# Performance work log

Hardware: AMD Instinct MI355X
Metric: run time of the kernel (lower is better)

## Reference

```python
import jax, jax.numpy as jnp
from jax import lax
import numpy as np

B, T, F, H, O = 4096, 2048, 8, 32, 8


def setup_inputs() -> dict:
    key = jax.random.key(0)
    k = jax.random.split(key, 7)
    s = 1.0 / np.sqrt(H).astype(np.float32)  # torch RNN/Linear init bound
    x = jax.random.normal(k[0], (B, T, F), dtype=jnp.float32)
    W_ih = jax.random.uniform(k[1], (H, F), minval=-s, maxval=s, dtype=jnp.float32)
    W_hh = jax.random.uniform(k[2], (H, H), minval=-s, maxval=s, dtype=jnp.float32)
    b_ih = jax.random.uniform(k[3], (H,), minval=-s, maxval=s, dtype=jnp.float32)
    b_hh = jax.random.uniform(k[4], (H,), minval=-s, maxval=s, dtype=jnp.float32)
    W_out = jax.random.uniform(k[5], (O, H), minval=-s, maxval=s, dtype=jnp.float32)
    b_out = jax.random.uniform(k[6], (O,), minval=-s, maxval=s, dtype=jnp.float32)
    return {"x": x, "W_ih": W_ih, "W_hh": W_hh, "b_ih": b_ih, "b_hh": b_hh,
            "W_out": W_out, "b_out": b_out}


def reference(x, W_ih, W_hh, b_ih, b_hh, W_out, b_out):
    # Precompute input projection for all timesteps: [B, T, H]
    xp = jnp.einsum('btf,hf->bth', x, W_ih) + b_ih + b_hh
    h0 = jnp.zeros((x.shape[0], W_hh.shape[0]), dtype=x.dtype)

    def step(h, xt):  # xt: [B, H]
        h = jnp.tanh(xt + h @ W_hh.T)
        return h, None

    h_final, _ = lax.scan(step, h0, jnp.swapaxes(xp, 0, 1))  # scan over T
    # torch returns out(h) with h of shape [num_layers=1, B, H]
    y = h_final @ W_out.T + b_out  # [B, O]
    return y[None]  # [1, B, O]
```

## Files before the change

### kernel.cpp

```cpp
#include <hip/hip_runtime.h>


typedef float v2f __attribute__((ext_vector_type(2)));

static constexpr int T_STEPS = 2048;
static constexpr int FDIM    = 8;
static constexpr int HDIM    = 32;
static constexpr int ODIM    = 8;
static constexpr int ROWS_PER_BLOCK = 8;
static constexpr int GROUP   = 4;
static constexpr int NGROUP  = T_STEPS / GROUP;
static constexpr int LSTR    = 36;

__global__ __launch_bounds__(256, 2) void rnn_scan_kernel(
    const float* __restrict__ x,
    const float* __restrict__ W_ih,
    const float* __restrict__ W_hh,
    const float* __restrict__ b_ih,
    const float* __restrict__ b_hh,
    const float* __restrict__ W_out,
    const float* __restrict__ b_out,
    float* __restrict__ out)
{
    const float K = 2.8853900817779268f;
    const int tid  = threadIdx.x;
    const int lane = tid & 63;
    const int wave = tid >> 6;
    const int q    = lane & 31;
    const int sub  = lane >> 5;
    const int r    = wave * 2 + sub;
    const long long b = (long long)blockIdx.x * ROWS_PER_BLOCK + r;

    __shared__ float hsh[ROWS_PER_BLOCK][LSTR];

    v2f wh[16];
    const float* whr = W_hh + q * HDIM;
#pragma unroll
    for (int i = 0; i < 16; ++i) {
        v2f w; w[0] = whr[2 * i] * K; w[1] = whr[2 * i + 1] * K; wh[i] = w;
    }
    v2f wiv[4];
    const float* wir = W_ih + q * FDIM;
#pragma unroll
    for (int i = 0; i < 4; ++i) {
        v2f w; w[0] = wir[2 * i] * K; w[1] = wir[2 * i + 1] * K; wiv[i] = w;
    }
    const float bias = (b_ih[q] + b_hh[q]) * K;

    hsh[r][q] = 0.0f;

    const float4* xq = reinterpret_cast<const float4*>(x + (size_t)b * T_STEPS * FDIM);
    const float4* hp = reinterpret_cast<const float4*>(&hsh[r][0]);
    float* hw = &hsh[r][q];

#define LOADG(buf, gi)                                                         \
    {                                                                          \
        const int base = (gi) * (2 * GROUP);                                   \
        _Pragma("unroll")                                                      \
        for (int k = 0; k < 2 * GROUP; ++k) buf[k] = xq[base + k];             \
    }                                                                          \
    asm volatile("" ::: "memory");

#define STEP(xa, xb)                                                           \
    {                                                                          \
        float4 g0 = hp[0], g1 = hp[1], g2 = hp[2], g3 = hp[3];                 \
        float4 g4 = hp[4], g5 = hp[5], g6 = hp[6], g7 = hp[7];                 \
        v2f a0; a0[0] = bias; a0[1] = 0.0f;                                    \
        v2f a1 = {0.0f, 0.0f}, a2 = {0.0f, 0.0f}, a3 = {0.0f, 0.0f};           \
        v2f t;                                                                 \
        t[0] = xa.x; t[1] = xa.y;  a0 = __builtin_elementwise_fma(wiv[0], t, a0); \
        t[0] = xa.z; t[1] = xa.w;  a1 = __builtin_elementwise_fma(wiv[1], t, a1); \
        t[0] = xb.x; t[1] = xb.y;  a2 = __builtin_elementwise_fma(wiv[2], t, a2); \
        t[0] = xb.z; t[1] = xb.w;  a3 = __builtin_elementwise_fma(wiv[3], t, a3); \
        t[0] = g0.x; t[1] = g0.y;  a0 = __builtin_elementwise_fma(wh[0],  t, a0); \
        t[0] = g0.z; t[1] = g0.w;  a1 = __builtin_elementwise_fma(wh[1],  t, a1); \
        t[0] = g1.x; t[1] = g1.y;  a2 = __builtin_elementwise_fma(wh[2],  t, a2); \
        t[0] = g1.z; t[1] = g1.w;  a3 = __builtin_elementwise_fma(wh[3],  t, a3); \
        t[0] = g2.x; t[1] = g2.y;  a0 = __builtin_elementwise_fma(wh[4],  t, a0); \
        t[0] = g2.z; t[1] = g2.w;  a1 = __builtin_elementwise_fma(wh[5],  t, a1); \
        t[0] = g3.x; t[1] = g3.y;  a2 = __builtin_elementwise_fma(wh[6],  t, a2); \
        t[0] = g3.z; t[1] = g3.w;  a3 = __builtin_elementwise_fma(wh[7],  t, a3); \
        t[0] = g4.x; t[1] = g4.y;  a0 = __builtin_elementwise_fma(wh[8],  t, a0); \
        t[0] = g4.z; t[1] = g4.w;  a1 = __builtin_elementwise_fma(wh[9],  t, a1); \
        t[0] = g5.x; t[1] = g5.y;  a2 = __builtin_elementwise_fma(wh[10], t, a2); \
        t[0] = g5.z; t[1] = g5.w;  a3 = __builtin_elementwise_fma(wh[11], t, a3); \
        t[0] = g6.x; t[1] = g6.y;  a0 = __builtin_elementwise_fma(wh[12], t, a0); \
        t[0] = g6.z; t[1] = g6.w;  a1 = __builtin_elementwise_fma(wh[13], t, a1); \
        t[0] = g7.x; t[1] = g7.y;  a2 = __builtin_elementwise_fma(wh[14], t, a2); \
        t[0] = g7.z; t[1] = g7.w;  a3 = __builtin_elementwise_fma(wh[15], t, a3); \
        v2f s01 = a0 + a1, s23 = a2 + a3;                                      \
        v2f st  = s01 + s23;                                                   \
        float s = st[0] + st[1];                                               \
        float e = __builtin_amdgcn_exp2f(s);                                   \
        float rc = __builtin_amdgcn_rcpf(e + 1.0f);                            \
        *hw = fmaf(-2.0f, rc, 1.0f);                                           \
    }

#define STEPS(buf)                                                             \
    STEP(buf[0], buf[1]) STEP(buf[2], buf[3])                                  \
    STEP(buf[4], buf[5]) STEP(buf[6], buf[7])

    float4 bufA[2 * GROUP], bufB[2 * GROUP];
    LOADG(bufA, 0)

    for (int g = 0; g < NGROUP; g += 2) {
        LOADG(bufB, g + 1)
        STEPS(bufA)
        {
            const int gn = (g + 2 < NGROUP) ? (g + 2) : (NGROUP - 1);
            LOADG(bufA, gn)
        }
        STEPS(bufB)
    }
#undef STEPS
#undef STEP
#undef LOADG

    __syncthreads();
    if (tid < ROWS_PER_BLOCK * ODIM) {
        const int rr = tid >> 3;
        const int o  = tid & 7;
        float acc = b_out[o];
#pragma unroll
        for (int j = 0; j < HDIM; ++j)
            acc = fmaf(hsh[rr][j], W_out[o * HDIM + j], acc);
        out[((long long)blockIdx.x * ROWS_PER_BLOCK + rr) * ODIM + o] = acc;
    }
}

extern "C" void kernel_launch(void* const* d_in, const int* in_sizes, int n_in,
                              void* d_out, int out_size, void* d_ws, size_t ws_size,
                              hipStream_t stream) {
    const float* x     = (const float*)d_in[0];
    const float* W_ih  = (const float*)d_in[1];
    const float* W_hh  = (const float*)d_in[2];
    const float* b_ih  = (const float*)d_in[3];
    const float* b_hh  = (const float*)d_in[4];
    const float* W_out = (const float*)d_in[5];
    const float* b_out = (const float*)d_in[6];

    const int B = in_sizes[0] / (T_STEPS * FDIM);
    const int grid = B / ROWS_PER_BLOCK;

    rnn_scan_kernel<<<grid, 256, 0, stream>>>(
        x, W_ih, W_hh, b_ih, b_hh, W_out, b_out, (float*)d_out);
}
```

Baseline: 687.0 us.

## Use fp16 hidden state with fdot2 and split-K lanes with swizzle reduction

Stores the hidden state in LDS as fp16 and computes the recurrent matvec with packed fp16 dot2 instructions. The work is remapped so each lane computes two output rows over half of K, and the two halves are combined with a ds_swizzle cross-lane exchange. Each lane now loads half the x inputs. The aim is fewer per-step VALU ops and LDS bytes on the serial critical path. In exchange the weights and hidden state lose precision, and the swizzle adds latency to every step.

```diff
diff --git a/kernel.cpp b/kernel.cpp
--- a/kernel.cpp
+++ b/kernel.cpp
@@ -2,6 +2,7 @@
 
 
 typedef float v2f __attribute__((ext_vector_type(2)));
+typedef _Float16 h2v __attribute__((ext_vector_type(2)));
 
 static constexpr int T_STEPS = 2048;
 static constexpr int FDIM    = 8;
@@ -10,7 +11,14 @@
 static constexpr int ROWS_PER_BLOCK = 8;
 static constexpr int GROUP   = 4;
 static constexpr int NGROUP  = T_STEPS / GROUP;
-static constexpr int LSTR    = 36;
+static constexpr int LSTR    = 40;
+
+__device__ __forceinline__ float fdot2(h2v a, h2v b, float c) {
+    return __builtin_amdgcn_fdot2(a, b, c, false);
+}
+__device__ __forceinline__ h2v bch(unsigned u) {
+    return __builtin_bit_cast(h2v, u);
+}
 
 __global__ __launch_bounds__(256, 2) void rnn_scan_kernel(
     const float* __restrict__ x,
@@ -26,88 +34,91 @@
     const int tid  = threadIdx.x;
     const int lane = tid & 63;
     const int wave = tid >> 6;
-    const int q    = lane & 31;
+    const int g    = lane & 15;
+    const int c    = (lane >> 4) & 1;
     const int sub  = lane >> 5;
     const int r    = wave * 2 + sub;
     const long long b = (long long)blockIdx.x * ROWS_PER_BLOCK + r;
+    const int d0 = 2 * g, d1 = 2 * g + 1;
 
-    __shared__ float hsh[ROWS_PER_BLOCK][LSTR];
+    __shared__ _Float16 hsh[ROWS_PER_BLOCK][LSTR];
 
-    v2f wh[16];
-    const float* whr = W_hh + q * HDIM;
+    h2v wA[8], wB[8];
+    const float* whr0 = W_hh + d0 * HDIM + 16 * c;
+    const float* whr1 = W_hh + d1 * HDIM + 16 * c;
 #pragma unroll
-    for (int i = 0; i < 16; ++i) {
-        v2f w; w[0] = whr[2 * i] * K; w[1] = whr[2 * i + 1] * K; wh[i] = w;
+    for (int j = 0; j < 8; ++j) {
+        h2v wa; wa[0] = (_Float16)(whr0[2 * j] * K); wa[1] = (_Float16)(whr0[2 * j + 1] * K);
+        wA[j] = wa;
+        h2v wb; wb[0] = (_Float16)(whr1[2 * j] * K); wb[1] = (_Float16)(whr1[2 * j + 1] * K);
+        wB[j] = wb;
     }
     v2f wiv[4];
-    const float* wir = W_ih + q * FDIM;
 #pragma unroll
-    for (int i = 0; i < 4; ++i) {
-        v2f w; w[0] = wir[2 * i] * K; w[1] = wir[2 * i + 1] * K; wiv[i] = w;
+    for (int f = 0; f < 4; ++f) {
+        v2f w; w[0] = W_ih[d0 * FDIM + 4 * c + f] * K;
+               w[1] = W_ih[d1 * FDIM + 4 * c + f] * K;
+        wiv[f] = w;
     }
-    const float bias = (b_ih[q] + b_hh[q]) * K;
+    v2f bias2;
+    bias2[0] = c ? 0.0f : (b_ih[d0] + b_hh[d0]) * K;
+    bias2[1] = c ? 0.0f : (b_ih[d1] + b_hh[d1]) * K;
 
-    hsh[r][q] = 0.0f;
+    hsh[r][2 * g + c] = (_Float16)0.0f;
 
     const float4* xq = reinterpret_cast<const float4*>(x + (size_t)b * T_STEPS * FDIM);
-    const float4* hp = reinterpret_cast<const float4*>(&hsh[r][0]);
-    float* hw = &hsh[r][q];
+    const uint4* hq = reinterpret_cast<const uint4*>(
+        reinterpret_cast<const char*>(&hsh[r][0]) + 32 * c);
+    _Float16* hw = &hsh[r][2 * g + c];
 
 #define LOADG(buf, gi)                                                         \
     {                                                                          \
-        const int base = (gi) * (2 * GROUP);                                   \
+        const int base = (gi) * (2 * GROUP) + c;                               \
         _Pragma("unroll")                                                      \
-        for (int k = 0; k < 2 * GROUP; ++k) buf[k] = xq[base + k];             \
+        for (int k = 0; k < GROUP; ++k) buf[k] = xq[base + 2 * k];             \
     }                                                                          \
     asm volatile("" ::: "memory");
 
-#define STEP(xa, xb)                                                           \
+#define STEP(xr)                                                               \
     {                                                                          \
-        float4 g0 = hp[0], g1 = hp[1], g2 = hp[2], g3 = hp[3];                 \
-        float4 g4 = hp[4], g5 = hp[5], g6 = hp[6], g7 = hp[7];                 \
-        v2f a0; a0[0] = bias; a0[1] = 0.0f;                                    \
-        v2f a1 = {0.0f, 0.0f}, a2 = {0.0f, 0.0f}, a3 = {0.0f, 0.0f};           \
+        uint4 u0 = hq[0], u1 = hq[1];                                          \
+        float c00 = 0.0f, c01 = 0.0f, c10 = 0.0f, c11 = 0.0f;                  \
+        c00 = fdot2(wA[0], bch(u0.x), c00);  c10 = fdot2(wB[0], bch(u0.x), c10); \
+        c01 = fdot2(wA[4], bch(u1.x), c01);  c11 = fdot2(wB[4], bch(u1.x), c11); \
+        c00 = fdot2(wA[1], bch(u0.y), c00);  c10 = fdot2(wB[1], bch(u0.y), c10); \
+        c01 = fdot2(wA[5], bch(u1.y), c01);  c11 = fdot2(wB[5], bch(u1.y), c11); \
+        c00 = fdot2(wA[2], bch(u0.z), c00);  c10 = fdot2(wB[2], bch(u0.z), c10); \
+        c01 = fdot2(wA[6], bch(u1.z), c01);  c11 = fdot2(wB[6], bch(u1.z), c11); \
+        c00 = fdot2(wA[3], bch(u0.w), c00);  c10 = fdot2(wB[3], bch(u0.w), c10); \
+        c01 = fdot2(wA[7], bch(u1.w), c01);  c11 = fdot2(wB[7], bch(u1.w), c11); \
+        v2f a = bias2;                                                         \
         v2f t;                                                                 \
-        t[0] = xa.x; t[1] = xa.y;  a0 = __builtin_elementwise_fma(wiv[0], t, a0); \
-        t[0] = xa.z; t[1] = xa.w;  a1 = __builtin_elementwise_fma(wiv[1], t, a1); \
-        t[0] = xb.x; t[1] = xb.y;  a2 = __builtin_elementwise_fma(wiv[2], t, a2); \
-        t[0] = xb.z; t[1] = xb.w;  a3 = __builtin_elementwise_fma(wiv[3], t, a3); \
-        t[0] = g0.x; t[1] = g0.y;  a0 = __builtin_elementwise_fma(wh[0],  t, a0); \
-        t[0] = g0.z; t[1] = g0.w;  a1 = __builtin_elementwise_fma(wh[1],  t, a1); \
-        t[0] = g1.x; t[1] = g1.y;  a2 = __builtin_elementwise_fma(wh[2],  t, a2); \
-        t[0] = g1.z; t[1] = g1.w;  a3 = __builtin_elementwise_fma(wh[3],  t, a3); \
-        t[0] = g2.x; t[1] = g2.y;  a0 = __builtin_elementwise_fma(wh[4],  t, a0); \
-        t[0] = g2.z; t[1] = g2.w;  a1 = __builtin_elementwise_fma(wh[5],  t, a1); \
-        t[0] = g3.x; t[1] = g3.y;  a2 = __builtin_elementwise_fma(wh[6],  t, a2); \
-        t[0] = g3.z; t[1] = g3.w;  a3 = __builtin_elementwise_fma(wh[7],  t, a3); \
-        t[0] = g4.x; t[1] = g4.y;  a0 = __builtin_elementwise_fma(wh[8],  t, a0); \
-        t[0] = g4.z; t[1] = g4.w;  a1 = __builtin_elementwise_fma(wh[9],  t, a1); \
-        t[0] = g5.x; t[1] = g5.y;  a2 = __builtin_elementwise_fma(wh[10], t, a2); \
-        t[0] = g5.z; t[1] = g5.w;  a3 = __builtin_elementwise_fma(wh[11], t, a3); \
-        t[0] = g6.x; t[1] = g6.y;  a0 = __builtin_elementwise_fma(wh[12], t, a0); \
-        t[0] = g6.z; t[1] = g6.w;  a1 = __builtin_elementwise_fma(wh[13], t, a1); \
-        t[0] = g7.x; t[1] = g7.y;  a2 = __builtin_elementwise_fma(wh[14], t, a2); \
-        t[0] = g7.z; t[1] = g7.w;  a3 = __builtin_elementwise_fma(wh[15], t, a3); \
-        v2f s01 = a0 + a1, s23 = a2 + a3;                                      \
-        v2f st  = s01 + s23;                                                   \
-        float s = st[0] + st[1];                                               \
+        t[0] = xr.x; t[1] = xr.x;  a = __builtin_elementwise_fma(wiv[0], t, a); \
+        t[0] = xr.y; t[1] = xr.y;  a = __builtin_elementwise_fma(wiv[1], t, a); \
+        t[0] = xr.z; t[1] = xr.z;  a = __builtin_elementwise_fma(wiv[2], t, a); \
+        t[0] = xr.w; t[1] = xr.w;  a = __builtin_elementwise_fma(wiv[3], t, a); \
+        v2f dotv; dotv[0] = c00 + c01; dotv[1] = c10 + c11;                    \
+        v2f s2 = a + dotv;                                                     \
+        float o0 = __int_as_float(__builtin_amdgcn_ds_swizzle(                 \
+                       __float_as_int(s2[0]), 0x401f));                        \
+        float o1 = __int_as_float(__builtin_amdgcn_ds_swizzle(                 \
+                       __float_as_int(s2[1]), 0x401f));                        \
+        float s = c ? (s2[1] + o1) : (s2[0] + o0);                             \
         float e = __builtin_amdgcn_exp2f(s);                                   \
         float rc = __builtin_amdgcn_rcpf(e + 1.0f);                            \
-        *hw = fmaf(-2.0f, rc, 1.0f);                                           \
+        *hw = (_Float16)fmaf(-2.0f, rc, 1.0f);                                 \
     }
 
-#define STEPS(buf)                                                             \
-    STEP(buf[0], buf[1]) STEP(buf[2], buf[3])                                  \
-    STEP(buf[4], buf[5]) STEP(buf[6], buf[7])
+#define STEPS(buf) STEP(buf[0]) STEP(buf[1]) STEP(buf[2]) STEP(buf[3])
 
-    float4 bufA[2 * GROUP], bufB[2 * GROUP];
+    float4 bufA[GROUP], bufB[GROUP];
     LOADG(bufA, 0)
 
-    for (int g = 0; g < NGROUP; g += 2) {
-        LOADG(bufB, g + 1)
+    for (int gi = 0; gi < NGROUP; gi += 2) {
+        LOADG(bufB, gi + 1)
         STEPS(bufA)
         {
-            const int gn = (g + 2 < NGROUP) ? (g + 2) : (NGROUP - 1);
+            const int gn = (gi + 2 < NGROUP) ? (gi + 2) : (NGROUP - 1);
             LOADG(bufA, gn)
         }
         STEPS(bufB)
@@ -123,7 +134,7 @@
         float acc = b_out[o];
 #pragma unroll
         for (int j = 0; j < HDIM; ++j)
-            acc = fmaf(hsh[rr][j], W_out[o * HDIM + j], acc);
+            acc = fmaf((float)hsh[rr][j], W_out[o * HDIM + j], acc);
         out[((long long)blockIdx.x * ROWS_PER_BLOCK + rr) * ODIM + o] = acc;
     }
 }
```

After: 643.1 us. 6.4% less time.

## Broadcast hidden state via ds_swizzle instead of LDS round-trip each step

Applied to the files above, without the earlier changes.

Keeps the hidden state in a register and gathers all 32 hidden values each step with ds_swizzle broadcast patterns within 32-lane groups, replacing the shared-memory write and vector reads of the state. This is meant to shorten the serial per-step dependency chain through LDS. It trades 8 vector LDS reads for 32 swizzle ops per step and drops packed v2f FMAs for scalar FMAs, which may cost more issue slots.

```diff
diff --git a/kernel.cpp b/kernel.cpp
--- a/kernel.cpp
+++ b/kernel.cpp
@@ -1,7 +1,5 @@
 #include <hip/hip_runtime.h>
 
-
-typedef float v2f __attribute__((ext_vector_type(2)));
 
 static constexpr int T_STEPS = 2048;
 static constexpr int FDIM    = 8;
@@ -10,7 +8,6 @@
 static constexpr int ROWS_PER_BLOCK = 8;
 static constexpr int GROUP   = 4;
 static constexpr int NGROUP  = T_STEPS / GROUP;
-static constexpr int LSTR    = 36;
 
 __global__ __launch_bounds__(256, 2) void rnn_scan_kernel(
     const float* __restrict__ x,
@@ -31,27 +28,18 @@
     const int r    = wave * 2 + sub;
     const long long b = (long long)blockIdx.x * ROWS_PER_BLOCK + r;
 
-    __shared__ float hsh[ROWS_PER_BLOCK][LSTR];
+    __shared__ float hsh[ROWS_PER_BLOCK][HDIM];
 
-    v2f wh[16];
-    const float* whr = W_hh + q * HDIM;
+    float wh[HDIM];
 #pragma unroll
-    for (int i = 0; i < 16; ++i) {
-        v2f w; w[0] = whr[2 * i] * K; w[1] = whr[2 * i + 1] * K; wh[i] = w;
-    }
-    v2f wiv[4];
-    const float* wir = W_ih + q * FDIM;
+    for (int j = 0; j < HDIM; ++j) wh[j] = W_hh[q * HDIM + j] * K;
+    float wi[FDIM];
 #pragma unroll
-    for (int i = 0; i < 4; ++i) {
-        v2f w; w[0] = wir[2 * i] * K; w[1] = wir[2 * i + 1] * K; wiv[i] = w;
-    }
+    for (int f = 0; f < FDIM; ++f) wi[f] = W_ih[q * FDIM + f] * K;
     const float bias = (b_ih[q] + b_hh[q]) * K;
 
-    hsh[r][q] = 0.0f;
-
     const float4* xq = reinterpret_cast<const float4*>(x + (size_t)b * T_STEPS * FDIM);
-    const float4* hp = reinterpret_cast<const float4*>(&hsh[r][0]);
-    float* hw = &hsh[r][q];
+    float h = 0.0f;
 
 #define LOADG(buf, gi)                                                         \
     {                                                                          \
@@ -61,39 +49,41 @@
     }                                                                          \
     asm volatile("" ::: "memory");
 
+#define SWZ(j) const float g##j = __int_as_float(                              \
+        __builtin_amdgcn_ds_swizzle(__float_as_int(h), ((j) << 5)));
+
 #define STEP(xa, xb)                                                           \
     {                                                                          \
-        float4 g0 = hp[0], g1 = hp[1], g2 = hp[2], g3 = hp[3];                 \
-        float4 g4 = hp[4], g5 = hp[5], g6 = hp[6], g7 = hp[7];                 \
-        v2f a0; a0[0] = bias; a0[1] = 0.0f;                                    \
-        v2f a1 = {0.0f, 0.0f}, a2 = {0.0f, 0.0f}, a3 = {0.0f, 0.0f};           \
-        v2f t;                                                                 \
-        t[0] = xa.x; t[1] = xa.y;  a0 = __builtin_elementwise_fma(wiv[0], t, a0); \
-        t[0] = xa.z; t[1] = xa.w;  a1 = __builtin_elementwise_fma(wiv[1], t, a1); \
-        t[0] = xb.x; t[1] = xb.y;  a2 = __builtin_elementwise_fma(wiv[2], t, a2); \
-        t[0] = xb.z; t[1] = xb.w;  a3 = __builtin_elementwise_fma(wiv[3], t, a3); \
-        t[0] = g0.x; t[1] = g0.y;  a0 = __builtin_elementwise_fma(wh[0],  t, a0); \
-        t[0] = g0.z; t[1] = g0.w;  a1 = __builtin_elementwise_fma(wh[1],  t, a1); \
-        t[0] = g1.x; t[1] = g1.y;  a2 = __builtin_elementwise_fma(wh[2],  t, a2); \
-        t[0] = g1.z; t[1] = g1.w;  a3 = __builtin_elementwise_fma(wh[3],  t, a3); \
-        t[0] = g2.x; t[1] = g2.y;  a0 = __builtin_elementwise_fma(wh[4],  t, a0); \
-        t[0] = g2.z; t[1] = g2.w;  a1 = __builtin_elementwise_fma(wh[5],  t, a1); \
-        t[0] = g3.x; t[1] = g3.y;  a2 = __builtin_elementwise_fma(wh[6],  t, a2); \
-        t[0] = g3.z; t[1] = g3.w;  a3 = __builtin_elementwise_fma(wh[7],  t, a3); \
-        t[0] = g4.x; t[1] = g4.y;  a0 = __builtin_elementwise_fma(wh[8],  t, a0); \
-        t[0] = g4.z; t[1] = g4.w;  a1 = __builtin_elementwise_fma(wh[9],  t, a1); \
-        t[0] = g5.x; t[1] = g5.y;  a2 = __builtin_elementwise_fma(wh[10], t, a2); \
-        t[0] = g5.z; t[1] = g5.w;  a3 = __builtin_elementwise_fma(wh[11], t, a3); \
-        t[0] = g6.x; t[1] = g6.y;  a0 = __builtin_elementwise_fma(wh[12], t, a0); \
-        t[0] = g6.z; t[1] = g6.w;  a1 = __builtin_elementwise_fma(wh[13], t, a1); \
-        t[0] = g7.x; t[1] = g7.y;  a2 = __builtin_elementwise_fma(wh[14], t, a2); \
-        t[0] = g7.z; t[1] = g7.w;  a3 = __builtin_elementwise_fma(wh[15], t, a3); \
-        v2f s01 = a0 + a1, s23 = a2 + a3;                                      \
-        v2f st  = s01 + s23;                                                   \
-        float s = st[0] + st[1];                                               \
-        float e = __builtin_amdgcn_exp2f(s);                                   \
-        float rc = __builtin_amdgcn_rcpf(e + 1.0f);                            \
-        *hw = fmaf(-2.0f, rc, 1.0f);                                           \
+        SWZ(0)  SWZ(1)  SWZ(2)  SWZ(3)  SWZ(4)  SWZ(5)  SWZ(6)  SWZ(7)         \
+        SWZ(8)  SWZ(9)  SWZ(10) SWZ(11) SWZ(12) SWZ(13) SWZ(14) SWZ(15)        \
+        SWZ(16) SWZ(17) SWZ(18) SWZ(19) SWZ(20) SWZ(21) SWZ(22) SWZ(23)        \
+        SWZ(24) SWZ(25) SWZ(26) SWZ(27) SWZ(28) SWZ(29) SWZ(30) SWZ(31)        \
+             \
+        float a0 = bias, a1 = 0.0f, a2 = 0.0f, a3 = 0.0f;                      \
+        a0 = fmaf(wi[0], xa.x, a0);  a1 = fmaf(wi[1], xa.y, a1);               \
+        a2 = fmaf(wi[2], xa.z, a2);  a3 = fmaf(wi[3], xa.w, a3);               \
+        a0 = fmaf(wi[4], xb.x, a0);  a1 = fmaf(wi[5], xb.y, a1);               \
+        a2 = fmaf(wi[6], xb.z, a2);  a3 = fmaf(wi[7], xb.w, a3);               \
+        a0 = fmaf(wh[0],  g0,  a0);  a1 = fmaf(wh[1],  g1,  a1);               \
+        a2 = fmaf(wh[2],  g2,  a2);  a3 = fmaf(wh[3],  g3,  a3);               \
+        a0 = fmaf(wh[4],  g4,  a0);  a1 = fmaf(wh[5],  g5,  a1);               \
+        a2 = fmaf(wh[6],  g6,  a2);  a3 = fmaf(wh[7],  g7,  a3);               \
+        a0 = fmaf(wh[8],  g8,  a0);  a1 = fmaf(wh[9],  g9,  a1);               \
+        a2 = fmaf(wh[10], g10, a2);  a3 = fmaf(wh[11], g11, a3);               \
+        a0 = fmaf(wh[12], g12, a0);  a1 = fmaf(wh[13], g13, a1);               \
+        a2 = fmaf(wh[14], g14, a2);  a3 = fmaf(wh[15], g15, a3);               \
+        a0 = fmaf(wh[16], g16, a0);  a1 = fmaf(wh[17], g17, a1);               \
+        a2 = fmaf(wh[18], g18, a2);  a3 = fmaf(wh[19], g19, a3);               \
+        a0 = fmaf(wh[20], g20, a0);  a1 = fmaf(wh[21], g21, a1);               \
+        a2 = fmaf(wh[22], g22, a2);  a3 = fmaf(wh[23], g23, a3);               \
+        a0 = fmaf(wh[24], g24, a0);  a1 = fmaf(wh[25], g25, a1);               \
+        a2 = fmaf(wh[26], g26, a2);  a3 = fmaf(wh[27], g27, a3);               \
+        a0 = fmaf(wh[28], g28, a0);  a1 = fmaf(wh[29], g29, a1);               \
+        a2 = fmaf(wh[30], g30, a2);  a3 = fmaf(wh[31], g31, a3);               \
+        const float s = (a0 + a1) + (a2 + a3);                                 \
+        const float e = __builtin_amdgcn_exp2f(s);                             \
+        const float rc = __builtin_amdgcn_rcpf(e + 1.0f);                      \
+        h = fmaf(-2.0f, rc, 1.0f);                                             \
     }
 
 #define STEPS(buf)                                                             \
@@ -103,19 +93,20 @@
     float4 bufA[2 * GROUP], bufB[2 * GROUP];
     LOADG(bufA, 0)
 
-    for (int g = 0; g < NGROUP; g += 2) {
-        LOADG(bufB, g + 1)
+    for (int gi = 0; gi < NGROUP; gi += 2) {
+        const int g1 = (gi + 1 < NGROUP) ? (gi + 1) : gi;
+        LOADG(bufB, g1)
         STEPS(bufA)
-        {
-            const int gn = (g + 2 < NGROUP) ? (g + 2) : (NGROUP - 1);
-            LOADG(bufA, gn)
-        }
+        const int g2 = (gi + 2 < NGROUP) ? (gi + 2) : gi;
+        LOADG(bufA, g2)
         STEPS(bufB)
     }
 #undef STEPS
 #undef STEP
+#undef SWZ
 #undef LOADG
 
+    hsh[r][q] = h;
     __syncthreads();
     if (tid < ROWS_PER_BLOCK * ODIM) {
         const int rr = tid >> 3;
```

Measured after the change: 962.5 us. 40.1% more time.
